# Kernel optimization log

Measured on AMD Instinct MI355X. Metric: run time of the kernel, lower is better.

## Reference

```python
import jax, jax.numpy as jnp
import numpy as np

DIM = 384
HEADS = 8


def setup_inputs() -> dict:
    key = jax.random.key(0)
    ks = jax.random.split(key, 6)
    B, H, W = 8, 64, 64
    N, C = H * W, DIM
    s = 0.02  # init scale for weights
    return {
        "x": jax.random.normal(ks[0], (B, N, C), jnp.float32),
        # depthwise conv: OIHW with feature_group_count=C -> [C,1,3,3]
        "w_sr": jax.random.normal(ks[1], (C, 1, 3, 3), jnp.float32) * s,
        "b_sr": jax.random.normal(ks[2], (C,), jnp.float32) * s,
        "ln_g": jnp.ones((C,), jnp.float32),
        "ln_b": jnp.zeros((C,), jnp.float32),
        # linears stored [in, out] (torch stores [out,in]; random so equivalent)
        "w_qkv": jax.random.normal(ks[3], (C, 3 * C), jnp.float32) * s,
        "w_proj": jax.random.normal(ks[4], (C, C), jnp.float32) * s,
        "b_proj": jax.random.normal(ks[5], (C,), jnp.float32) * s,
        "H": 64,
        "W": 64,
    }


def reference(x, w_sr, b_sr, ln_g, ln_b, w_qkv, w_proj, b_proj, H, W):
    B, N, C = x.shape
    h = HEADS
    d = C // h
    shortcut = x

    # --- depthwise conv branch: sr(x) -> LN -> GELU -> residual add ---
    x_img = x.transpose(0, 2, 1).reshape(B, C, H, W)
    x_sr = jax.lax.conv_general_dilated(
        x_img, w_sr, window_strides=(1, 1), padding="SAME",
        dimension_numbers=("NCHW", "OIHW", "NCHW"), feature_group_count=C,
    ) + b_sr[None, :, None, None]
    x_sr = x_sr.reshape(B, C, N).transpose(0, 2, 1)  # [B, N, C]
    mu = x_sr.mean(-1, keepdims=True)
    var = x_sr.var(-1, keepdims=True)
    xn = (x_sr - mu) * jax.lax.rsqrt(var + 1e-5) * ln_g + ln_b
    x = x + jax.nn.gelu(xn, approximate=False)  # torch GELU is erf-based

    # --- linear attention ---
    qkv = (x @ w_qkv).reshape(B, N, 3, h, d)
    q = qkv[:, :, 0].transpose(0, 2, 1, 3)  # [B, h, N, d]
    k = qkv[:, :, 1].transpose(0, 2, 1, 3)
    v = qkv[:, :, 2].transpose(0, 2, 1, 3)
    q = jax.nn.softmax(q, axis=-2)  # softmax over sequence dim N
    k = jax.nn.softmax(k, axis=-1)  # softmax over head_dim
    ctx = jnp.einsum("bhnd,bhne->bhde", k, v)          # [B, h, d, d]
    attn = jnp.einsum("bhnd,bhde->bhne", q, ctx)       # [B, h, N, d]
    attn = attn.transpose(0, 2, 1, 3).reshape(B, N, C)

    out = attn @ w_proj + b_proj
    return out + shortcut
```

## Files before the change

kernel.cpp:

```cpp
#include <hip/hip_runtime.h>

typedef unsigned short u16;
typedef u16   u16x4  __attribute__((ext_vector_type(4)));
typedef u16   u16x8  __attribute__((ext_vector_type(8)));
typedef short short8 __attribute__((ext_vector_type(8)));
typedef float floatx4 __attribute__((ext_vector_type(4)));
typedef float f4     __attribute__((ext_vector_type(4)));

typedef const __attribute__((address_space(1))) unsigned gu32;
typedef __attribute__((address_space(3))) unsigned lu32;

#define BB 8
#define NN 4096
#define CC 384

__device__ __forceinline__ u16 f2bf(float f){
  unsigned u = __float_as_uint(f);
  u += 0x7FFFu + ((u >> 16) & 1u);
  return (u16)(u >> 16);
}

__global__ __launch_bounds__(384) void k_pre(
    const float* __restrict__ x, const float* __restrict__ w_sr, const float* __restrict__ b_sr,
    const float* __restrict__ ln_g, const float* __restrict__ ln_b,
    const float* __restrict__ wqkv, u16* __restrict__ xa16, u16* __restrict__ WT,
    float* __restrict__ Z)
{
  const int blk = blockIdx.x;

  if (blk >= 4204) {
    int off = (blk - 4204) * 1536 + ((int)threadIdx.x << 2);
    const f4 zz = {0.f, 0.f, 0.f, 0.f};
    *(f4*)(Z + off) = zz;
    return;
  }

  if (blk >= 4096) {
    const int pb = blk - 4096;
    const int cg = pb % 18, kg = pb / 18;
    const int c0 = cg << 6, k0 = kg << 6;
    const int tid = threadIdx.x;
    __shared__ u16 t[64][72];
    if (tid < 256) {
#pragma unroll
      for (int i = 0; i < 4; i++) {
        int idx = tid + (i << 8);
        int r = idx >> 4, c4 = (idx & 15) << 2;
        f4 v = *(const f4*)(wqkv + (size_t)(k0 + r) * 1152 + c0 + c4);
#pragma unroll
        for (int j = 0; j < 4; j++) t[c4 + j][r] = f2bf(v[j]);
      }
    }
    __syncthreads();
    if (tid < 256) {
#pragma unroll
      for (int i = 0; i < 2; i++) {
        int idx = tid + (i << 8);
        int c = idx >> 3, j = (idx & 7) << 3;
        *(u16x8*)(WT + (size_t)(c0 + c) * 384 + k0 + j) = *(const u16x8*)&t[c][j];
      }
    }
    return;
  }

  const int b = blk >> 9;
  const int hh = (blk >> 3) & 63;
  const int ww0 = (blk & 7) << 3;
  const int c = threadIdx.x;

  float wgt[9];
#pragma unroll
  for (int i = 0; i < 9; i++) wgt[i] = w_sr[c * 9 + i];
  const float lg = ln_g[c], lb = ln_b[c];
  const float bias = b_sr[c];

  float rowv[3][10];
#pragma unroll
  for (int r = 0; r < 3; r++) {
    int y = hh + r - 1;
    bool yok = (unsigned)y < 64u;
#pragma unroll
    for (int j = 0; j < 10; j++) {
      int xx = ww0 + j - 1;
      bool ok = yok && ((unsigned)xx < 64u);
      rowv[r][j] = ok ? x[((size_t)((b << 12) + (y << 6) + xx)) * CC + c] : 0.f;
    }
  }

  float acc[8];
#pragma unroll
  for (int p = 0; p < 8; p++) {
    float a = bias;
#pragma unroll
    for (int r = 0; r < 3; r++)
#pragma unroll
      for (int j = 0; j < 3; j++)
        a += rowv[r][p + j] * wgt[r * 3 + j];
    acc[p] = a;
  }

  __shared__ float ls1[6][8], ls2[6][8], mb[2][8];
  const int wid = threadIdx.x >> 6, lane = threadIdx.x & 63;
#pragma unroll
  for (int p = 0; p < 8; p++) {
    float s1 = acc[p], s2 = acc[p] * acc[p];
#pragma unroll
    for (int o = 32; o > 0; o >>= 1) { s1 += __shfl_down(s1, o); s2 += __shfl_down(s2, o); }
    if (lane == 0) { ls1[wid][p] = s1; ls2[wid][p] = s2; }
  }
  __syncthreads();
  if (threadIdx.x < 8) {
    int p = threadIdx.x;
    float a = 0.f, q = 0.f;
#pragma unroll
    for (int i = 0; i < 6; i++) { a += ls1[i][p]; q += ls2[i][p]; }
    float mean = a * (1.0f / CC);
    float var  = q * (1.0f / CC) - mean * mean;
    mb[0][p] = mean; mb[1][p] = rsqrtf(var + 1e-5f);
  }
  __syncthreads();
#pragma unroll
  for (int p = 0; p < 8; p++) {
    float xn = (acc[p] - mb[0][p]) * mb[1][p] * lg + lb;
    float g  = 0.5f * xn * (1.0f + erff(xn * 0.70710678118654752f));
    size_t pix = (size_t)(b << 12) + (hh << 6) + ww0 + p;
    xa16[pix * CC + c] = f2bf(rowv[1][p + 1] + g);
  }
}

__global__ __launch_bounds__(512) void k_qkv(
    const u16* __restrict__ xa16, const u16* __restrict__ WT, float* __restrict__ S,
    u16* __restrict__ K16T, u16* __restrict__ V16T, u16* __restrict__ P16)
{
  const int rt = blockIdx.x;
  const int g  = blockIdx.y;
  const int b  = rt >> 6;
  const int n0 = rt << 6;
  const int tid = threadIdx.x;
  const int wv = tid >> 6, lane = tid & 63, l15 = lane & 15, quad = lane >> 4;
  const int wc = wv;

  __shared__ __attribute__((aligned(16))) u16 lA[2][64][32];
  __shared__ __attribute__((aligned(16))) u16 lB[2][384][32];

  const u16* Bbase = WT + (size_t)((g == 2) ? 0 : (384 + g * 384)) * 384;
  const int sw8 = (quad ^ ((l15 >> 1) & 3)) << 3;

  floatx4 acc[12];
  const floatx4 z = {0.f, 0.f, 0.f, 0.f};
#pragma unroll
  for (int i = 0; i < 12; i++) acc[i] = z;

  auto stage = [&](int bi, int k0) {
    if (wv < 4) {
      int cl = (wv << 4) + (lane >> 2);
      int sc = ((lane & 3) ^ ((cl >> 1) & 3)) << 3;
      __builtin_amdgcn_global_load_lds((gu32*)(xa16 + (size_t)(n0 + cl) * 384 + k0 + sc),
                                       (lu32*)&lA[bi][wv << 4][0], 16, 0, 0);
    }
#pragma unroll
    for (int i = 0; i < 3; i++) {
      int j = wv * 3 + i;
      int cl = (j << 4) + (lane >> 2);
      int sc = ((lane & 3) ^ ((cl >> 1) & 3)) << 3;
      __builtin_amdgcn_global_load_lds((gu32*)(Bbase + (size_t)cl * 384 + k0 + sc),
                                       (lu32*)&lB[bi][j << 4][0], 16, 0, 0);
    }
  };

  stage(0, 0);

  for (int t = 0; t < 12; t++) {
    const int cur = t & 1;
    if (t < 11) {
      stage(cur ^ 1, (t + 1) << 5);
      if (wv < 4) asm volatile("s_waitcnt vmcnt(4)" ::: "memory");
      else        asm volatile("s_waitcnt vmcnt(3)" ::: "memory");
    } else {
      asm volatile("s_waitcnt vmcnt(0)" ::: "memory");
    }
    __builtin_amdgcn_s_barrier();
    short8 af[4], bf[3];
#pragma unroll
    for (int mi = 0; mi < 4; mi++) af[mi] = *(const short8*)&lA[cur][(mi << 4) + l15][sw8];
#pragma unroll
    for (int ni = 0; ni < 3; ni++) bf[ni] = *(const short8*)&lB[cur][wc * 48 + (ni << 4) + l15][sw8];
#pragma unroll
    for (int mi = 0; mi < 4; mi++)
#pragma unroll
      for (int ni = 0; ni < 3; ni++)
        acc[mi * 3 + ni] = __builtin_amdgcn_mfma_f32_16x16x32_bf16(af[mi], bf[ni], acc[mi * 3 + ni], 0, 0, 0);
    __builtin_amdgcn_s_barrier();
  }

  if (g == 0) {
#pragma unroll
    for (int mi = 0; mi < 4; mi++)
#pragma unroll
      for (int rr = 0; rr < 4; rr++) {
        float x0 = acc[mi * 3 + 0][rr], x1 = acc[mi * 3 + 1][rr], x2 = acc[mi * 3 + 2][rr];
        float m = fmaxf(fmaxf(x0, x1), x2);
#pragma unroll
        for (int o = 8; o >= 1; o >>= 1) m = fmaxf(m, __shfl_xor(m, o));
        float e0 = expf(x0 - m), e1 = expf(x1 - m), e2 = expf(x2 - m);
        float s = e0 + e1 + e2;
#pragma unroll
        for (int o = 8; o >= 1; o >>= 1) s += __shfl_xor(s, o);
        float inv = 1.0f / s;
        acc[mi * 3 + 0][rr] = e0 * inv; acc[mi * 3 + 1][rr] = e1 * inv; acc[mi * 3 + 2][rr] = e2 * inv;
      }
  }

  if (g == 2) {
#pragma unroll
    for (int ni = 0; ni < 3; ni++) {
      int col = wc * 48 + (ni << 4) + l15;
      float s = 0.f;
#pragma unroll
      for (int mi = 0; mi < 4; mi++) {
        int rowb = n0 + (mi << 4) + (quad << 2);
        float e0 = expf(acc[mi * 3 + ni][0]), e1 = expf(acc[mi * 3 + ni][1]);
        float e2 = expf(acc[mi * 3 + ni][2]), e3 = expf(acc[mi * 3 + ni][3]);
        P16[(size_t)(rowb + 0) * 384 + col] = f2bf(e0);
        P16[(size_t)(rowb + 1) * 384 + col] = f2bf(e1);
        P16[(size_t)(rowb + 2) * 384 + col] = f2bf(e2);
        P16[(size_t)(rowb + 3) * 384 + col] = f2bf(e3);
        s += e0 + e1 + e2 + e3;
      }
      s += __shfl_down(s, 32);
      s += __shfl_down(s, 16);
      if (lane < 16) atomicAdd(&S[b * 384 + wc * 48 + (ni << 4) + lane], s);
    }
  } else {
    u16* dst = g ? V16T : K16T;
    const int nl = ((rt & 63) << 6) + (quad << 2);
#pragma unroll
    for (int mi = 0; mi < 4; mi++)
#pragma unroll
      for (int ni = 0; ni < 3; ni++) {
        int hd = wc * 48 + (ni << 4) + l15;
        u16x4 v4 = { f2bf(acc[mi * 3 + ni][0]), f2bf(acc[mi * 3 + ni][1]),
                     f2bf(acc[mi * 3 + ni][2]), f2bf(acc[mi * 3 + ni][3]) };
        *(u16x4*)(dst + ((size_t)b * 384 + hd) * 4096 + nl + (mi << 4)) = v4;
      }
  }
}

__global__ __launch_bounds__(256) void k_ctx(
    const u16* __restrict__ K16T, const u16* __restrict__ V16T, float* __restrict__ ctx)
{
  const int bh = blockIdx.x;
  const int b = bh >> 3, h = bh & 7;
  const int n0 = blockIdx.y << 8;
  const int tid = threadIdx.x;
  const int wv = tid >> 6, lane = tid & 63, l15 = lane & 15, quad = lane >> 4;

  __shared__ __attribute__((aligned(16))) char smem[50688];
  u16 (*lkT)[264] = (u16(*)[264])smem;
  u16 (*lvT)[264] = (u16(*)[264])(smem + 25344);
  float (*pctx)[2304] = (float(*)[2304])smem;

#pragma unroll
  for (int i = 0; i < 6; i++) {
    int idx = tid + (i << 8);
    int d = idx >> 5, c8 = (idx & 31) << 3;
    *(u16x8*)&lkT[d][c8] = *(const u16x8*)(K16T + ((size_t)b * 384 + h * 48 + d) * 4096 + n0 + c8);
    *(u16x8*)&lvT[d][c8] = *(const u16x8*)(V16T + ((size_t)b * 384 + h * 48 + d) * 4096 + n0 + c8);
  }
  __syncthreads();

  floatx4 c2[9];
  const floatx4 z = {0.f, 0.f, 0.f, 0.f};
#pragma unroll
  for (int i = 0; i < 9; i++) c2[i] = z;
#pragma unroll
  for (int kk2 = 0; kk2 < 2; kk2++) {
    int rb = (wv << 6) + (kk2 << 5) + (quad << 3);
    short8 ak[3], av[3];
#pragma unroll
    for (int t = 0; t < 3; t++) {
      ak[t] = *(const short8*)&lkT[(t << 4) + l15][rb];
      av[t] = *(const short8*)&lvT[(t << 4) + l15][rb];
    }
#pragma unroll
    for (int dt = 0; dt < 3; dt++)
#pragma unroll
      for (int et = 0; et < 3; et++)
        c2[dt * 3 + et] = __builtin_amdgcn_mfma_f32_16x16x32_bf16(ak[dt], av[et], c2[dt * 3 + et], 0, 0, 0);
  }
  __syncthreads();

#pragma unroll
  for (int dt = 0; dt < 3; dt++)
#pragma unroll
    for (int et = 0; et < 3; et++)
#pragma unroll
      for (int rr = 0; rr < 4; rr++) {
        int d = (dt << 4) + (quad << 2) + rr;
        int e = (et << 4) + l15;
        pctx[wv][d * 48 + e] = c2[dt * 3 + et][rr];
      }
  __syncthreads();
#pragma unroll
  for (int i = 0; i < 9; i++) {
    int cell = tid + (i << 8);
    float s = pctx[0][cell] + pctx[1][cell] + pctx[2][cell] + pctx[3][cell];
    atomicAdd(&ctx[(size_t)bh * 2304 + cell], s);
  }
}

__global__ __launch_bounds__(256) void k_w2(
    const float* __restrict__ ctx, const float* __restrict__ S,
    const float* __restrict__ wp, u16* __restrict__ W2T)
{
  const int bh = blockIdx.x;
  const int b = bh >> 3, h = bh & 7;
  const int c0 = blockIdx.y << 7;
  const int tid = threadIdx.x;
  __shared__ float rs[48];
  __shared__ float c2[48][48];
  __shared__ float lwp[48][128];
  __shared__ u16 tr[128][48];
  if (tid < 48) rs[tid] = 1.0f / S[b * 384 + h * 48 + tid];
  __syncthreads();
#pragma unroll
  for (int i = 0; i < 9; i++) {
    int cell = tid + (i << 8);
    int d = cell / 48, e = cell - d * 48;
    c2[d][e] = ctx[(size_t)bh * 2304 + cell] * rs[d];
  }
#pragma unroll
  for (int i = 0; i < 24; i++) {
    int idx = tid + (i << 8);
    int e = idx >> 7, c = idx & 127;
    lwp[e][c] = wp[(size_t)(h * 48 + e) * 384 + c0 + c];
  }
  __syncthreads();
  const int c = tid & 127;
  const int dbase = tid >> 7;
#pragma unroll
  for (int it = 0; it < 24; it++) {
    int d = (it << 1) + dbase;
    float s = 0.f;
#pragma unroll
    for (int e = 0; e < 48; e++) s += c2[d][e] * lwp[e][c];
    tr[c][d] = f2bf(s);
  }
  __syncthreads();
  const int cc = tid >> 1, half = tid & 1;
#pragma unroll
  for (int i = 0; i < 3; i++) {
    u16x8 v = *(const u16x8*)&tr[cc][half * 24 + (i << 3)];
    *(u16x8*)(W2T + ((size_t)b * 384 + c0 + cc) * 384 + h * 48 + half * 24 + (i << 3)) = v;
  }
}

__global__ __launch_bounds__(512) void k_qproj(
    const u16* __restrict__ P16, const u16* __restrict__ W2T,
    const float* __restrict__ bias, const float* __restrict__ x, float* __restrict__ out)
{
  const int bm = blockIdx.x;
  const int b = bm >> 6;
  const int n0 = bm << 6;
  const int tid = threadIdx.x;
  const int wv = tid >> 6, lane = tid & 63, l15 = lane & 15, quad = lane >> 4;
  const int wc = wv;

  __shared__ __attribute__((aligned(16))) u16 lA[2][64][32];
  __shared__ __attribute__((aligned(16))) u16 lB[2][384][32];

  const u16* Bbase = W2T + (size_t)b * 384 * 384;
  const int sw8 = (quad ^ ((l15 >> 1) & 3)) << 3;

  floatx4 acc[12];
  const floatx4 z = {0.f, 0.f, 0.f, 0.f};
#pragma unroll
  for (int i = 0; i < 12; i++) acc[i] = z;

  auto stage = [&](int bi, int k0) {
    if (wv < 4) {
      int cl = (wv << 4) + (lane >> 2);
      int sc = ((lane & 3) ^ ((cl >> 1) & 3)) << 3;
      __builtin_amdgcn_global_load_lds((gu32*)(P16 + (size_t)(n0 + cl) * 384 + k0 + sc),
                                       (lu32*)&lA[bi][wv << 4][0], 16, 0, 0);
    }
#pragma unroll
    for (int i = 0; i < 3; i++) {
      int j = wv * 3 + i;
      int cl = (j << 4) + (lane >> 2);
      int sc = ((lane & 3) ^ ((cl >> 1) & 3)) << 3;
      __builtin_amdgcn_global_load_lds((gu32*)(Bbase + (size_t)cl * 384 + k0 + sc),
                                       (lu32*)&lB[bi][j << 4][0], 16, 0, 0);
    }
  };

  stage(0, 0);

  for (int t = 0; t < 12; t++) {
    const int cur = t & 1;
    if (t < 11) {
      stage(cur ^ 1, (t + 1) << 5);
      if (wv < 4) asm volatile("s_waitcnt vmcnt(4)" ::: "memory");
      else        asm volatile("s_waitcnt vmcnt(3)" ::: "memory");
    } else {
      asm volatile("s_waitcnt vmcnt(0)" ::: "memory");
    }
    __builtin_amdgcn_s_barrier();
    short8 af[4], bf[3];
#pragma unroll
    for (int mi = 0; mi < 4; mi++) af[mi] = *(const short8*)&lA[cur][(mi << 4) + l15][sw8];
#pragma unroll
    for (int ni = 0; ni < 3; ni++) bf[ni] = *(const short8*)&lB[cur][wc * 48 + (ni << 4) + l15][sw8];
#pragma unroll
    for (int mi = 0; mi < 4; mi++)
#pragma unroll
      for (int ni = 0; ni < 3; ni++)
        acc[mi * 3 + ni] = __builtin_amdgcn_mfma_f32_16x16x32_bf16(af[mi], bf[ni], acc[mi * 3 + ni], 0, 0, 0);
    __builtin_amdgcn_s_barrier();
  }

#pragma unroll
  for (int ni = 0; ni < 3; ni++) {
    int col = wc * 48 + (ni << 4) + l15;
    float bc = bias[col];
#pragma unroll
    for (int mi = 0; mi < 4; mi++) {
#pragma unroll
      for (int rr = 0; rr < 4; rr++) {
        int row = n0 + (mi << 4) + (quad << 2) + rr;
        out[(size_t)row * 384 + col] = acc[mi * 3 + ni][rr] + bc + x[(size_t)row * 384 + col];
      }
    }
  }
}

extern "C" void kernel_launch(void* const* d_in, const int* in_sizes, int n_in,
                              void* d_out, int out_size, void* d_ws, size_t ws_size,
                              hipStream_t stream)
{
  const float* x      = (const float*)d_in[0];
  const float* w_sr   = (const float*)d_in[1];
  const float* b_sr   = (const float*)d_in[2];
  const float* ln_g   = (const float*)d_in[3];
  const float* ln_b   = (const float*)d_in[4];
  const float* w_qkv  = (const float*)d_in[5];
  const float* w_proj = (const float*)d_in[6];
  const float* b_proj = (const float*)d_in[7];
  float* out = (float*)d_out;

  float* S   = (float*)d_ws;
  float* ctx = (float*)((char*)d_ws + 12288);
  u16*   WT  = (u16*)((char*)d_ws + 602112);
  u16*   W2T = (u16*)((char*)d_ws + 1486848);
  u16*   xa16= (u16*)((char*)d_ws + 3846144);
  u16*   P16 = (u16*)((char*)d_ws + 29011968);
  u16*   K16T= (u16*)d_out;
  u16*   V16T= (u16*)d_out + (size_t)8 * 384 * 4096;

  k_pre<<<4302, 384, 0, stream>>>(x, w_sr, b_sr, ln_g, ln_b, w_qkv, xa16, WT, (float*)d_ws);
  k_qkv<<<dim3(512, 3), 512, 0, stream>>>(xa16, WT, S, K16T, V16T, P16);
  k_ctx<<<dim3(64, 16), 256, 0, stream>>>(K16T, V16T, ctx);
  k_w2<<<dim3(64, 3), 256, 0, stream>>>(ctx, S, w_proj, W2T);
  k_qproj<<<512, 512, 0, stream>>>(P16, W2T, b_proj, x, out);
}
```

Measured before the change: 254.5 us.

## Vectorize depthwise conv/LN/GELU prologue over 4 channels with 32-pixel tiles

Restructures the conv+LayerNorm+GELU portion of k_pre so each thread handles 4 consecutive channels using float4 loads and bf16x4 stores. Each block now covers 32 pixels as 4 groups of 8 instead of 8 pixels, cutting the block count from 4096 to 1024. The LN reduction is reworked to reduce per group across shuffles and shared memory. The aim is to replace scalar 4-byte loads with wider loads and to amortize per-block overhead. In exchange each thread uses more registers, and the residual x is re-read from global memory instead of being kept in registers.

```diff
diff --git a/kernel.cpp b/kernel.cpp
--- a/kernel.cpp
+++ b/kernel.cpp
@@ -28,15 +28,15 @@
 {
   const int blk = blockIdx.x;
 
-  if (blk >= 4204) {
-    int off = (blk - 4204) * 1536 + ((int)threadIdx.x << 2);
+  if (blk >= 1132) {
+    int off = (blk - 1132) * 1536 + ((int)threadIdx.x << 2);
     const f4 zz = {0.f, 0.f, 0.f, 0.f};
     *(f4*)(Z + off) = zz;
     return;
   }
 
-  if (blk >= 4096) {
-    const int pb = blk - 4096;
+  if (blk >= 1024) {
+    const int pb = blk - 1024;
     const int cg = pb % 18, kg = pb / 18;
     const int c0 = cg << 6, k0 = kg << 6;
     const int tid = threadIdx.x;
@@ -63,68 +63,86 @@
     return;
   }
 
-  const int b = blk >> 9;
-  const int hh = (blk >> 3) & 63;
-  const int ww0 = (blk & 7) << 3;
-  const int c = threadIdx.x;
-
-  float wgt[9];
-#pragma unroll
-  for (int i = 0; i < 9; i++) wgt[i] = w_sr[c * 9 + i];
-  const float lg = ln_g[c], lb = ln_b[c];
-  const float bias = b_sr[c];
-
-  float rowv[3][10];
+  const int b = blk >> 7;
+  const int rem = blk & 127;
+  const int hh = rem >> 1;
+  const int ww0 = (rem & 1) << 5;
+  const int t = threadIdx.x;
+  const int g = t & 3;
+  const int cq = t >> 2;
+  const int c4 = cq << 2;
+
+  f4 wgt4[9];
+#pragma unroll
+  for (int i = 0; i < 9; i++) {
+    wgt4[i][0] = w_sr[(c4 + 0) * 9 + i];
+    wgt4[i][1] = w_sr[(c4 + 1) * 9 + i];
+    wgt4[i][2] = w_sr[(c4 + 2) * 9 + i];
+    wgt4[i][3] = w_sr[(c4 + 3) * 9 + i];
+  }
+  const f4 bias4 = *(const f4*)(b_sr + c4);
+  const f4 lg4   = *(const f4*)(ln_g + c4);
+  const f4 lb4   = *(const f4*)(ln_b + c4);
+
+  f4 acc4[8];
+#pragma unroll
+  for (int p = 0; p < 8; p++) acc4[p] = bias4;
+
+  const int colbase = ww0 + (g << 3) - 1;
+  const f4 z4 = {0.f, 0.f, 0.f, 0.f};
 #pragma unroll
   for (int r = 0; r < 3; r++) {
     int y = hh + r - 1;
     bool yok = (unsigned)y < 64u;
+    f4 rv[10];
 #pragma unroll
     for (int j = 0; j < 10; j++) {
-      int xx = ww0 + j - 1;
-      bool ok = yok && ((unsigned)xx < 64u);
-      rowv[r][j] = ok ? x[((size_t)((b << 12) + (y << 6) + xx)) * CC + c] : 0.f;
-    }
-  }
-
-  float acc[8];
+      int col = colbase + j;
+      bool ok = yok && ((unsigned)col < 64u);
+      rv[j] = ok ? *(const f4*)(x + (size_t)((b << 12) + (y << 6) + col) * 384 + c4) : z4;
+    }
+#pragma unroll
+    for (int p = 0; p < 8; p++)
+#pragma unroll
+      for (int j = 0; j < 3; j++)
+        acc4[p] += rv[p + j] * wgt4[r * 3 + j];
+  }
+
+  __shared__ float ls1[6][4][8], ls2[6][4][8], mb[2][4][8];
+  const int wid = t >> 6, lane = t & 63;
 #pragma unroll
   for (int p = 0; p < 8; p++) {
-    float a = bias;
-#pragma unroll
-    for (int r = 0; r < 3; r++)
-#pragma unroll
-      for (int j = 0; j < 3; j++)
-        a += rowv[r][p + j] * wgt[r * 3 + j];
-    acc[p] = a;
-  }
-
-  __shared__ float ls1[6][8], ls2[6][8], mb[2][8];
-  const int wid = threadIdx.x >> 6, lane = threadIdx.x & 63;
-#pragma unroll
-  for (int p = 0; p < 8; p++) {
-    float s1 = acc[p], s2 = acc[p] * acc[p];
-#pragma unroll
-    for (int o = 32; o > 0; o >>= 1) { s1 += __shfl_down(s1, o); s2 += __shfl_down(s2, o); }
-    if (lane == 0) { ls1[wid][p] = s1; ls2[wid][p] = s2; }
-  }
-  __syncthreads();
-  if (threadIdx.x < 8) {
-    int p = threadIdx.x;
+    f4 a = acc4[p];
+    float s1 = a[0] + a[1] + a[2] + a[3];
+    float s2 = a[0]*a[0] + a[1]*a[1] + a[2]*a[2] + a[3]*a[3];
+#pragma unroll
+    for (int o = 32; o >= 4; o >>= 1) { s1 += __shfl_down(s1, o); s2 += __shfl_down(s2, o); }
+    if (lane < 4) { ls1[wid][lane][p] = s1; ls2[wid][lane][p] = s2; }
+  }
+  __syncthreads();
+  if (t < 32) {
+    int g2 = t >> 3, p2 = t & 7;
     float a = 0.f, q = 0.f;
 #pragma unroll
-    for (int i = 0; i < 6; i++) { a += ls1[i][p]; q += ls2[i][p]; }
+    for (int w = 0; w < 6; w++) { a += ls1[w][g2][p2]; q += ls2[w][g2][p2]; }
     float mean = a * (1.0f / CC);
     float var  = q * (1.0f / CC) - mean * mean;
-    mb[0][p] = mean; mb[1][p] = rsqrtf(var + 1e-5f);
+    mb[0][g2][p2] = mean; mb[1][g2][p2] = rsqrtf(var + 1e-5f);
   }
   __syncthreads();
 #pragma unroll
   for (int p = 0; p < 8; p++) {
-    float xn = (acc[p] - mb[0][p]) * mb[1][p] * lg + lb;
-    float g  = 0.5f * xn * (1.0f + erff(xn * 0.70710678118654752f));
-    size_t pix = (size_t)(b << 12) + (hh << 6) + ww0 + p;
-    xa16[pix * CC + c] = f2bf(rowv[1][p + 1] + g);
+    float mean = mb[0][g][p], rs = mb[1][g][p];
+    size_t pix = (size_t)(b << 12) + (hh << 6) + ww0 + (g << 3) + p;
+    f4 xr = *(const f4*)(x + pix * 384 + c4);
+    u16x4 o;
+#pragma unroll
+    for (int k = 0; k < 4; k++) {
+      float xn = (acc4[p][k] - mean) * rs * lg4[k] + lb4[k];
+      float gl = 0.5f * xn * (1.0f + erff(xn * 0.70710678118654752f));
+      o[k] = f2bf(xr[k] + gl);
+    }
+    *(u16x4*)(xa16 + pix * 384 + c4) = o;
   }
 }
 
@@ -457,7 +475,7 @@
   u16*   K16T= (u16*)d_out;
   u16*   V16T= (u16*)d_out + (size_t)8 * 384 * 4096;
 
-  k_pre<<<4302, 384, 0, stream>>>(x, w_sr, b_sr, ln_g, ln_b, w_qkv, xa16, WT, (float*)d_ws);
+  k_pre<<<1230, 384, 0, stream>>>(x, w_sr, b_sr, ln_g, ln_b, w_qkv, xa16, WT, (float*)d_ws);
   k_qkv<<<dim3(512, 3), 512, 0, stream>>>(xa16, WT, S, K16T, V16T, P16);
   k_ctx<<<dim3(64, 16), 256, 0, stream>>>(K16T, V16T, ctx);
   k_w2<<<dim3(64, 3), 256, 0, stream>>>(ctx, S, w_proj, W2T);
```

Result: slower. 274.6 us (+7.9%).
